# Optimization experiments

Measured on AMD Instinct MI355X. Metric: run time of the kernel, lower is better.

The kernel has to match this reference:

```python
import jax, jax.numpy as jnp
import numpy as np

N_QUBITS = 10
DIM = 2 ** N_QUBITS
N_POINTS = 64
D_FEAT = 10
N_LAYERS = 5

# bit tables: bits[:, q] = q-th least-significant bit of the state index.
# kron order in the original builds angles[n-1] x ... x angles[0], so angle q acts on bit q.
_bits = ((np.arange(DIM)[:, None] >> np.arange(N_QUBITS)[None, :]) & 1).astype(np.float32)
BITS_C = jnp.asarray(_bits - 0.5)  # (DIM, n): b_q - 1/2 -> rz diag phase coeffs
# crz ring: crz_matrix(i+1,...) is diagonal phase exp(i*theta*b_{i}*(b_{i+1}-1/2)) (control i, target i+1);
# close_ring is control n-1, target 0.
_ctrl = np.concatenate([np.arange(N_QUBITS - 1), [N_QUBITS - 1]])
_tgt = np.concatenate([np.arange(1, N_QUBITS), [0]])
RING_COEF = jnp.asarray(_bits[:, _ctrl] * (_bits[:, _tgt] - 0.5))  # (DIM, n)
H_GATES = jnp.broadcast_to(
    jnp.asarray((np.array([[1, 1], [1, -1]]) / np.sqrt(2)).astype(np.complex64)),
    (N_QUBITS, 2, 2))


def rz_diag(x, start):
    # rz_layer kron order: qubit q gets angle x[(start + n-1-q) % d]; rz = diag(e^{-it/2}, e^{it/2})
    idx = (start + N_QUBITS - 1 - np.arange(N_QUBITS)) % D_FEAT
    return jnp.exp(1j * (BITS_C @ x[idx]))  # (DIM,) complex64


def ring_diag(angles):
    return jnp.exp(1j * (RING_COEF @ angles))  # (DIM,) complex64


def ry_gates(angles):
    c, s = jnp.cos(0.5 * angles), jnp.sin(0.5 * angles)
    # (n, 2, 2): [[c, -s], [s, c]]
    return jnp.stack([jnp.stack([c, -s], -1), jnp.stack([s, c], -1)], -2).astype(jnp.complex64)


def apply_1q(state, gates):
    # apply gates[q] (2x2) to qubit q (axis n-1-q of the (2,)*n reshaped state)
    psi = state.reshape((2,) * N_QUBITS)
    for q in range(N_QUBITS):
        ax = N_QUBITS - 1 - q
        psi = jnp.moveaxis(jnp.tensordot(gates[q], psi, axes=([1], [ax])), 0, ax)
    return psi.reshape(DIM)


def block_f(state, x, bp, start):
    state = apply_1q(state, H_GATES)
    state = state * rz_diag(x, start)
    state = apply_1q(state, ry_gates(bp[0]))
    return state * ring_diag(bp[1])


def adj_block_f(state, x, bp, start):
    state = state * jnp.conj(ring_diag(bp[1]))
    state = apply_1q(state, ry_gates(-bp[0]))  # ry(t)^dagger = ry(-t)
    state = state * jnp.conj(rz_diag(x, start))
    return apply_1q(state, H_GATES)  # H is self-adjoint


def pair_prob(x1, x2, params):
    state = jnp.zeros((DIM,), jnp.complex64).at[0].set(1.0)
    for j in range(N_LAYERS):
        state = block_f(state, x1, params[j], j * N_QUBITS)
    for k in range(N_LAYERS):
        # faithful to original: start = (num_q - k - 1) * num_q (uses num_q, not n_layers)
        state = adj_block_f(state, x2, params[N_LAYERS - 1 - k], (N_QUBITS - k - 1) * N_QUBITS)
    a = state[0]
    return jnp.real(a) ** 2 + jnp.imag(a) ** 2  # |<0|U2^dag U1|0>|^2


def _kta(data, labels, params):
    x1 = jnp.repeat(data, N_POINTS, axis=0)   # point i of each pair
    x2 = jnp.tile(data, (N_POINTS, 1))        # point j of each pair
    k = jax.vmap(pair_prob, in_axes=(0, 0, None))(x1, x2, params)  # (N*N,)
    lm = (labels[:, None] * labels[None, :]).reshape(-1)
    kp = jnp.sum(lm * k)
    return kp / jnp.sqrt(jnp.sum(k * k) * jnp.sum(lm * lm))


def setup_inputs() -> dict:
    key = jax.random.key(0)
    k1, k2, k3 = jax.random.split(key, 3)
    data = jax.random.normal(k1, (N_POINTS, D_FEAT), jnp.float32)
    labels = jnp.where(jax.random.normal(k2, (N_POINTS,)) >= 0, 1.0, -1.0).astype(jnp.float32)
    params = jax.random.uniform(k3, (N_LAYERS, 2, N_QUBITS), jnp.float32, 0.0, 2.0 * np.pi)
    return {"data": data, "labels": labels, "params": params}


def reference(data, labels, params):
    return _kta(data, labels, params)
```

## Files before the change

kernel.cpp:

```cpp
#include <hip/hip_runtime.h>
#include <math.h>

#define NQ 10
#define DIM 1024
#define NPTS 64
#define DFEAT 10
#define NLAYERS 5
#define NPAIR 2080
#define GBLK  (NPAIR / 4)

#define IS2 0.70710678118654752440f

#define PART_OFF ((size_t)NPTS * DIM * sizeof(float2))

__global__ __launch_bounds__(1024) void state_kernel(
    const float* __restrict__ data,
    const float* __restrict__ params,
    float2* __restrict__ psi)
{
    const int i    = blockIdx.x;
    const int tid  = threadIdx.x;
    const int lane = tid & 63;

    __shared__ float4 mc[NLAYERS][NQ];
    __shared__ float2 xbuf[DIM];

    if (tid < NLAYERS * NQ) {
        const int L = tid / NQ, q = tid - L * NQ;
        const float xh = 0.5f * data[i * DFEAT + (9 - q)];
        const float cx = __cosf(xh), sx = __sinf(xh);
        float c = 1.f, s = 0.f;
        if (L != NLAYERS - 1) {
            const float th = 0.5f * params[L * 2 * NQ + q];
            c = __cosf(th); s = __sinf(th);
        }
        const float p = (c + s) * IS2, qm = (c - s) * IS2;
        mc[L][q] = make_float4(qm * cx, -p * sx, p * cx, -qm * sx);
    }
    __syncthreads();

    float re, im;
    {
        float Pr = 1.f, Pi = 0.f;
#pragma unroll 1
        for (int q = 0; q < NQ; ++q) {
            const float4 m = mc[0][q];
            const int b = (tid >> q) & 1;
            const float fr = b ? m.z : m.x;
            const float fi = b ? -m.w : m.y;
            const float nr = Pr * fr - Pi * fi;
            const float ni = Pr * fi + Pi * fr;
            Pr = nr; Pi = ni;
        }
        re = Pr; im = Pi;
    }

#pragma unroll 1
    for (int L = 0; L < NLAYERS; ++L) {
        if (L > 0) {
#pragma unroll 1
            for (int q = 0; q < 6; ++q) {
                const float4 m = mc[L][q];
                const int   b = (lane >> q) & 1;
                const float msr = b ? -m.x : m.x;
                const float msi = m.y;
                const float mpr = m.z;
                const float mpi = b ? -m.w : m.w;
                const float pr = __shfl_xor(re, 1 << q, 64);
                const float pi = __shfl_xor(im, 1 << q, 64);
                const float nr = msr * re - msi * im + mpr * pr - mpi * pi;
                const float ni = msr * im + msi * re + mpr * pi + mpi * pr;
                re = nr; im = ni;
            }
#pragma unroll 1
            for (int q = 6; q < NQ; ++q) {
                const float4 m = mc[L][q];
                const int   b = (tid >> q) & 1;
                const float msr = b ? -m.x : m.x;
                const float msi = m.y;
                const float mpr = m.z;
                const float mpi = b ? -m.w : m.w;
                xbuf[tid] = make_float2(re, im);
                __syncthreads();
                const float2 p2 = xbuf[tid ^ (1 << q)];
                const float nr = msr * re - msi * im + mpr * p2.x - mpi * p2.y;
                const float ni = msr * im + msi * re + mpr * p2.y + mpi * p2.x;
                re = nr; im = ni;
                __syncthreads();
            }
        }

        if (L < NLAYERS - 1) {
            const float* rg = params + L * 2 * NQ + NQ;
            float ph = 0.f;
#pragma unroll 1
            for (int n = 0; n < NQ; ++n) {
                const int   nn = (n == 9) ? 0 : (n + 1);
                const float g  = rg[n];
                const float t  = (((tid >> nn) & 1) ? 0.5f : -0.5f) * g;
                ph += ((tid >> n) & 1) ? t : 0.f;
            }
            const float s = __sinf(ph), c = __cosf(ph);
            const float nr = re * c - im * s;
            const float ni = re * s + im * c;
            re = nr; im = ni;
        }
    }

    psi[i * DIM + tid] = make_float2(re, im);
}

__global__ __launch_bounds__(256) void gram_kernel(
    const float4* __restrict__ psi4,
    const float* __restrict__ labels,
    float* __restrict__ partials)
{
    __shared__ float sm[2][4];
    const int wave = threadIdx.x >> 6;
    const int lane = threadIdx.x & 63;
    const int w    = blockIdx.x * 4 + wave;

    int i = (int)((129.0f - sqrtf(16641.0f - 8.0f * (float)w)) * 0.5f);
    int Ci = 64 * i - ((i * (i - 1)) >> 1);
    while (w < Ci)            { --i; Ci = 64 * i - ((i * (i - 1)) >> 1); }
    while (w >= Ci + 64 - i)  { Ci += 64 - i; ++i; }
    const int j = i + (w - Ci);

    const float4* a = psi4 + i * (DIM / 2);
    const float4* b = psi4 + j * (DIM / 2);

    float zr = 0.f, zi = 0.f;
#pragma unroll
    for (int r = 0; r < 8; ++r) {
        const int k = (r << 6) | lane;
        const float4 av = a[k], bv = b[k];
        zr += bv.x * av.x + bv.y * av.y + bv.z * av.z + bv.w * av.w;
        zi += bv.x * av.y - bv.y * av.x + bv.z * av.w - bv.w * av.z;
    }
#pragma unroll
    for (int off = 32; off; off >>= 1) {
        zr += __shfl_xor(zr, off, 64);
        zi += __shfl_xor(zi, off, 64);
    }

    if (lane == 0) {
        const float k = zr * zr + zi * zi;
        const float wgt = (i == j) ? 1.f : 2.f;
        sm[0][wave] = wgt * labels[i] * labels[j] * k;
        sm[1][wave] = wgt * k * k;
    }
    __syncthreads();
    if (threadIdx.x == 0) {
        partials[2 * blockIdx.x]     = sm[0][0] + sm[0][1] + sm[0][2] + sm[0][3];
        partials[2 * blockIdx.x + 1] = sm[1][0] + sm[1][1] + sm[1][2] + sm[1][3];
    }
}

__global__ __launch_bounds__(256) void reduce_kernel(
    const float* __restrict__ partials,
    const float* __restrict__ labels,
    float* __restrict__ out)
{
    __shared__ float sm[3][4];
    const int tid  = threadIdx.x;
    const int lane = tid & 63;
    const int wave = tid >> 6;

    float slk = 0.f, skk = 0.f, sl2 = 0.f;
    for (int p = tid; p < GBLK; p += 256) {
        slk += partials[2 * p];
        skk += partials[2 * p + 1];
    }
    if (tid < NPTS) { const float l = labels[tid]; sl2 = l * l; }

#pragma unroll
    for (int off = 32; off; off >>= 1) {
        slk += __shfl_xor(slk, off, 64);
        skk += __shfl_xor(skk, off, 64);
        sl2 += __shfl_xor(sl2, off, 64);
    }
    if (lane == 0) { sm[0][wave] = slk; sm[1][wave] = skk; sm[2][wave] = sl2; }
    __syncthreads();
    if (tid == 0) {
        const float a = sm[0][0] + sm[0][1] + sm[0][2] + sm[0][3];
        const float b = sm[1][0] + sm[1][1] + sm[1][2] + sm[1][3];
        const float c = sm[2][0] + sm[2][1] + sm[2][2] + sm[2][3];
        out[0] = a / sqrtf(b * (c * c));
    }
}

extern "C" void kernel_launch(void* const* d_in, const int* in_sizes, int n_in,
                              void* d_out, int out_size, void* d_ws, size_t ws_size,
                              hipStream_t stream) {
    const float* data   = (const float*)d_in[0];
    const float* labels = (const float*)d_in[1];
    const float* params = (const float*)d_in[2];
    float* out = (float*)d_out;

    float2* psi      = (float2*)d_ws;
    float*  partials = (float*)((char*)d_ws + PART_OFF);

    state_kernel <<<NPTS, 1024, 0, stream>>>(data, params, psi);
    gram_kernel  <<<GBLK,  256, 0, stream>>>((const float4*)psi, labels, partials);
    reduce_kernel<<<1,     256, 0, stream>>>(partials, labels, out);
}
```

Measured before the change: 73.89 us.

## Permute state layout via LDS transpose so all qubit gates use wave shuffles

Replaces the four per-qubit LDS exchanges (each with two barriers) for high qubits with a single bit-permuting transpose through shared memory per layer, after which every qubit becomes a lane-local shuffle. The layout alternates between identity and a swizzled index ordering across layers, with ring phases computed on the permuted index. It cuts barriers and LDS traffic in the state kernel but adds index bookkeeping and XOR-swizzled addressing to avoid bank conflicts.

```diff
diff --git a/kernel.cpp b/kernel.cpp
--- a/kernel.cpp
+++ b/kernel.cpp
@@ -13,6 +13,24 @@
 
 #define PART_OFF ((size_t)NPTS * DIM * sizeof(float2))
 
+__device__ __forceinline__ void ring_rot(float& re, float& im,
+                                         const float* __restrict__ rg,
+                                         int idx)
+{
+    float ph = 0.f;
+#pragma unroll 1
+    for (int n = 0; n < NQ; ++n) {
+        const int   nn = (n == 9) ? 0 : (n + 1);
+        const float g  = rg[n];
+        const float t  = (((idx >> nn) & 1) ? 0.5f : -0.5f) * g;
+        ph += ((idx >> n) & 1) ? t : 0.f;
+    }
+    const float s = __sinf(ph), c = __cosf(ph);
+    const float nr = re * c - im * s;
+    const float ni = re * s + im * c;
+    re = nr; im = ni;
+}
+
 __global__ __launch_bounds__(1024) void state_kernel(
     const float* __restrict__ data,
     const float* __restrict__ params,
@@ -20,10 +38,13 @@
 {
     const int i    = blockIdx.x;
     const int tid  = threadIdx.x;
-    const int lane = tid & 63;
 
     __shared__ float4 mc[NLAYERS][NQ];
     __shared__ float2 xbuf[DIM];
+
+    const int sig    = (tid & 0x030) | ((tid & 0x00F) << 6) | ((tid >> 6) & 0x00F);
+    const int aw_id  = tid ^ ((tid >> 6) & 0xF);
+    const int aw_sig = sig ^ (tid & 0xF);
 
     if (tid < NLAYERS * NQ) {
         const int L = tid / NQ, q = tid - L * NQ;
@@ -54,56 +75,37 @@
         }
         re = Pr; im = Pi;
     }
-
-#pragma unroll 1
-    for (int L = 0; L < NLAYERS; ++L) {
-        if (L > 0) {
-#pragma unroll 1
-            for (int q = 0; q < 6; ++q) {
-                const float4 m = mc[L][q];
-                const int   b = (lane >> q) & 1;
-                const float msr = b ? -m.x : m.x;
-                const float msi = m.y;
-                const float mpr = m.z;
-                const float mpi = b ? -m.w : m.w;
-                const float pr = __shfl_xor(re, 1 << q, 64);
-                const float pi = __shfl_xor(im, 1 << q, 64);
-                const float nr = msr * re - msi * im + mpr * pr - mpi * pi;
-                const float ni = msr * im + msi * re + mpr * pi + mpi * pr;
-                re = nr; im = ni;
-            }
-#pragma unroll 1
-            for (int q = 6; q < NQ; ++q) {
-                const float4 m = mc[L][q];
-                const int   b = (tid >> q) & 1;
-                const float msr = b ? -m.x : m.x;
-                const float msi = m.y;
-                const float mpr = m.z;
-                const float mpi = b ? -m.w : m.w;
-                xbuf[tid] = make_float2(re, im);
+    ring_rot(re, im, params + NQ, tid);
+
+#pragma unroll 1
+    for (int L = 1; L < NLAYERS; ++L) {
+        const int ph = (L - 1) & 1;
+#pragma unroll 1
+        for (int s = 0; s < NQ; ++s) {
+            if (s == 6) {
+                xbuf[ph ? aw_sig : aw_id] = make_float2(re, im);
                 __syncthreads();
-                const float2 p2 = xbuf[tid ^ (1 << q)];
-                const float nr = msr * re - msi * im + mpr * p2.x - mpi * p2.y;
-                const float ni = msr * im + msi * re + mpr * p2.y + mpi * p2.x;
-                re = nr; im = ni;
+                const float2 v = xbuf[ph ? aw_id : aw_sig];
+                re = v.x; im = v.y;
                 __syncthreads();
             }
-        }
-
+            int q, lb;
+            if (ph == 0) { q = s;                      lb = (s < 6) ? s : s - 6; }
+            else         { q = (s < 6) ? s + 4 : s - 6; lb = (q >= 6) ? q - 6 : q; }
+            const float4 m = mc[L][q];
+            const int   b = (tid >> lb) & 1;
+            const float msr = b ? -m.x : m.x;
+            const float msi = m.y;
+            const float mpr = m.z;
+            const float mpi = b ? -m.w : m.w;
+            const float pr = __shfl_xor(re, 1 << lb, 64);
+            const float pi = __shfl_xor(im, 1 << lb, 64);
+            const float nr = msr * re - msi * im + mpr * pr - mpi * pi;
+            const float ni = msr * im + msi * re + mpr * pi + mpi * pr;
+            re = nr; im = ni;
+        }
         if (L < NLAYERS - 1) {
-            const float* rg = params + L * 2 * NQ + NQ;
-            float ph = 0.f;
-#pragma unroll 1
-            for (int n = 0; n < NQ; ++n) {
-                const int   nn = (n == 9) ? 0 : (n + 1);
-                const float g  = rg[n];
-                const float t  = (((tid >> nn) & 1) ? 0.5f : -0.5f) * g;
-                ph += ((tid >> n) & 1) ? t : 0.f;
-            }
-            const float s = __sinf(ph), c = __cosf(ph);
-            const float nr = re * c - im * s;
-            const float ni = re * s + im * c;
-            re = nr; im = ni;
+            ring_rot(re, im, params + L * 2 * NQ + NQ, (ph == 0) ? sig : tid);
         }
     }
 
```

Measured after the change: 76.58 us. +3.6%, slower.

## Fuse state, gram and reduce kernels into one cooperative launch with grid syncs

Applied to the files above, without the earlier changes.

Merges the three kernels into a single cooperative kernel of 64 blocks of 1024 threads. Grid-wide syncs separate the state-vector construction, the pairwise overlap stage and the final reduction. This removes two kernel launches and their inter-kernel gaps. In exchange, the gram stage runs on only 64 blocks (1024 waves) instead of 520 smaller blocks, and it pays the cost of grid barriers.

```diff
diff --git a/kernel.cpp b/kernel.cpp
--- a/kernel.cpp
+++ b/kernel.cpp
@@ -1,5 +1,8 @@
 #include <hip/hip_runtime.h>
+#include <hip/hip_cooperative_groups.h>
 #include <math.h>
+
+namespace cg = cooperative_groups;
 
 #define NQ 10
 #define DIM 1024
@@ -7,23 +10,31 @@
 #define DFEAT 10
 #define NLAYERS 5
 #define NPAIR 2080
-#define GBLK  (NPAIR / 4)
+#define NWAVES_G (NPTS * 16)
 
 #define IS2 0.70710678118654752440f
 
 #define PART_OFF ((size_t)NPTS * DIM * sizeof(float2))
 
-__global__ __launch_bounds__(1024) void state_kernel(
+__global__ __launch_bounds__(1024) void kta_kernel(
     const float* __restrict__ data,
+    const float* __restrict__ labels,
     const float* __restrict__ params,
-    float2* __restrict__ psi)
+    float2* __restrict__ psi,
+    float* __restrict__ partials,
+    float* __restrict__ out)
 {
+    cg::grid_group grid = cg::this_grid();
+
     const int i    = blockIdx.x;
     const int tid  = threadIdx.x;
     const int lane = tid & 63;
+    const int wave = tid >> 6;
 
     __shared__ float4 mc[NLAYERS][NQ];
     __shared__ float2 xbuf[DIM];
+    __shared__ float  gsum[2][16];
+
 
     if (tid < NLAYERS * NQ) {
         const int L = tid / NQ, q = tid - L * NQ;
@@ -108,84 +119,67 @@
     }
 
     psi[i * DIM + tid] = make_float2(re, im);
-}
-
-__global__ __launch_bounds__(256) void gram_kernel(
-    const float4* __restrict__ psi4,
-    const float* __restrict__ labels,
-    float* __restrict__ partials)
-{
-    __shared__ float sm[2][4];
-    const int wave = threadIdx.x >> 6;
-    const int lane = threadIdx.x & 63;
-    const int w    = blockIdx.x * 4 + wave;
-
-    int i = (int)((129.0f - sqrtf(16641.0f - 8.0f * (float)w)) * 0.5f);
-    int Ci = 64 * i - ((i * (i - 1)) >> 1);
-    while (w < Ci)            { --i; Ci = 64 * i - ((i * (i - 1)) >> 1); }
-    while (w >= Ci + 64 - i)  { Ci += 64 - i; ++i; }
-    const int j = i + (w - Ci);
-
-    const float4* a = psi4 + i * (DIM / 2);
-    const float4* b = psi4 + j * (DIM / 2);
-
-    float zr = 0.f, zi = 0.f;
-#pragma unroll
-    for (int r = 0; r < 8; ++r) {
-        const int k = (r << 6) | lane;
-        const float4 av = a[k], bv = b[k];
-        zr += bv.x * av.x + bv.y * av.y + bv.z * av.z + bv.w * av.w;
-        zi += bv.x * av.y - bv.y * av.x + bv.z * av.w - bv.w * av.z;
-    }
-#pragma unroll
-    for (int off = 32; off; off >>= 1) {
-        zr += __shfl_xor(zr, off, 64);
-        zi += __shfl_xor(zi, off, 64);
-    }
-
-    if (lane == 0) {
-        const float k = zr * zr + zi * zi;
-        const float wgt = (i == j) ? 1.f : 2.f;
-        sm[0][wave] = wgt * labels[i] * labels[j] * k;
-        sm[1][wave] = wgt * k * k;
-    }
-    __syncthreads();
-    if (threadIdx.x == 0) {
-        partials[2 * blockIdx.x]     = sm[0][0] + sm[0][1] + sm[0][2] + sm[0][3];
-        partials[2 * blockIdx.x + 1] = sm[1][0] + sm[1][1] + sm[1][2] + sm[1][3];
-    }
-}
-
-__global__ __launch_bounds__(256) void reduce_kernel(
-    const float* __restrict__ partials,
-    const float* __restrict__ labels,
-    float* __restrict__ out)
-{
-    __shared__ float sm[3][4];
-    const int tid  = threadIdx.x;
-    const int lane = tid & 63;
-    const int wave = tid >> 6;
-
-    float slk = 0.f, skk = 0.f, sl2 = 0.f;
-    for (int p = tid; p < GBLK; p += 256) {
-        slk += partials[2 * p];
-        skk += partials[2 * p + 1];
-    }
-    if (tid < NPTS) { const float l = labels[tid]; sl2 = l * l; }
-
-#pragma unroll
-    for (int off = 32; off; off >>= 1) {
-        slk += __shfl_xor(slk, off, 64);
-        skk += __shfl_xor(skk, off, 64);
-        sl2 += __shfl_xor(sl2, off, 64);
-    }
-    if (lane == 0) { sm[0][wave] = slk; sm[1][wave] = skk; sm[2][wave] = sl2; }
+
+    grid.sync();
+
+    const float4* __restrict__ psi4 = (const float4*)psi;
+    float bslk = 0.f, bskk = 0.f;
+    const int gw = blockIdx.x * 16 + wave;
+
+#pragma unroll 1
+    for (int p = gw; p < NPAIR; p += NWAVES_G) {
+        int a = (int)((129.0f - sqrtf(16641.0f - 8.0f * (float)p)) * 0.5f);
+        int Ca = 64 * a - ((a * (a - 1)) >> 1);
+        while (p < Ca)            { --a; Ca = 64 * a - ((a * (a - 1)) >> 1); }
+        while (p >= Ca + 64 - a)  { Ca += 64 - a; ++a; }
+        const int b = a + (p - Ca);
+
+        const float4* __restrict__ pa = psi4 + a * (DIM / 2);
+        const float4* __restrict__ pb = psi4 + b * (DIM / 2);
+
+        float zr = 0.f, zi = 0.f;
+#pragma unroll
+        for (int r = 0; r < 8; ++r) {
+            const int k = (r << 6) | lane;
+            const float4 av = pa[k], bv = pb[k];
+            zr += bv.x * av.x + bv.y * av.y + bv.z * av.z + bv.w * av.w;
+            zi += bv.x * av.y - bv.y * av.x + bv.z * av.w - bv.w * av.z;
+        }
+#pragma unroll
+        for (int off = 32; off; off >>= 1) {
+            zr += __shfl_xor(zr, off, 64);
+            zi += __shfl_xor(zi, off, 64);
+        }
+        const float k   = zr * zr + zi * zi;
+        const float wgt = (a == b) ? 1.f : 2.f;
+        bslk += wgt * labels[a] * labels[b] * k;
+        bskk += wgt * k * k;
+    }
+
+    if (lane == 0) { gsum[0][wave] = bslk; gsum[1][wave] = bskk; }
     __syncthreads();
     if (tid == 0) {
-        const float a = sm[0][0] + sm[0][1] + sm[0][2] + sm[0][3];
-        const float b = sm[1][0] + sm[1][1] + sm[1][2] + sm[1][3];
-        const float c = sm[2][0] + sm[2][1] + sm[2][2] + sm[2][3];
-        out[0] = a / sqrtf(b * (c * c));
+        float s0 = 0.f, s1 = 0.f;
+#pragma unroll
+        for (int w = 0; w < 16; ++w) { s0 += gsum[0][w]; s1 += gsum[1][w]; }
+        partials[2 * blockIdx.x]     = s0;
+        partials[2 * blockIdx.x + 1] = s1;
+    }
+
+    grid.sync();
+
+    if (blockIdx.x == 0 && tid < 64) {
+        float slk = partials[2 * tid];
+        float skk = partials[2 * tid + 1];
+        const float l = labels[tid];
+        float sl2 = l * l;
+#pragma unroll
+        for (int off = 32; off; off >>= 1) {
+            slk += __shfl_xor(slk, off, 64);
+            skk += __shfl_xor(skk, off, 64);
+            sl2 += __shfl_xor(sl2, off, 64);
+        }
+        if (tid == 0) out[0] = slk / sqrtf(skk * (sl2 * sl2));
     }
 }
 
@@ -200,7 +194,8 @@
     float2* psi      = (float2*)d_ws;
     float*  partials = (float*)((char*)d_ws + PART_OFF);
 
-    state_kernel <<<NPTS, 1024, 0, stream>>>(data, params, psi);
-    gram_kernel  <<<GBLK,  256, 0, stream>>>((const float4*)psi, labels, partials);
-    reduce_kernel<<<1,     256, 0, stream>>>(partials, labels, out);
+    void* args[] = { (void*)&data, (void*)&labels, (void*)&params,
+                     (void*)&psi, (void*)&partials, (void*)&out };
+    hipLaunchCooperativeKernel((const void*)kta_kernel,
+                               dim3(NPTS), dim3(1024), args, 0, stream);
 }
```

New measurement: 108.3 us. 46.6% more time.
